# Kernel tuning notes

Hardware: AMD Instinct MI355X
Metric: run time of the kernel (lower is better)

The kernel has to match this reference:

```python
import jax, jax.numpy as jnp
import numpy as np
from jax import lax


def setup_inputs() -> dict:
    key = jax.random.key(0)
    k1, k2 = jax.random.split(key)
    x = jax.random.normal(k1, (16, 224, 224, 256), dtype=jnp.float32)
    # Conv2D(1, 7): kernel HWIO [7,7,2,1], glorot-ish scale
    conv_w = jax.random.normal(k2, (7, 7, 2, 1), dtype=jnp.float32) * 0.1
    conv_b = jnp.zeros((1,), dtype=jnp.float32)
    return {"x": x, "conv_w": conv_w, "conv_b": conv_b}


def reference(x, conv_w, conv_b):
    # channel-wise stats: [B,H,W,1] each
    max_pool = jnp.max(x, axis=-1, keepdims=True)
    avg_pool = jnp.mean(x, axis=-1, keepdims=True)
    concat = jnp.concatenate([max_pool, avg_pool], axis=-1)  # [B,H,W,2]
    attn = lax.conv_general_dilated(
        concat, conv_w,
        window_strides=(1, 1), padding='SAME',
        dimension_numbers=('NHWC', 'HWIO', 'NHWC'))
    attn = jax.nn.sigmoid(attn + conv_b)  # [B,H,W,1]
    return x * attn
```

## Files before the change

kernel.cpp:

```cpp
#include <hip/hip_runtime.h>
#include <math.h>

#define B_ 16
#define H_ 224
#define W_ 224
#define C_ 256
#define NPIX (B_*H_*W_)
#define NROW (B_*H_)

typedef float f32x4 __attribute__((ext_vector_type(4)));

__global__ __launch_bounds__(256) void pool_kernel(const float* __restrict__ x,
                                                   float2* __restrict__ pooled) {
    const int t    = threadIdx.x;
    const int wave = t >> 6;
    const int lane = t & 63;
    const int grp  = lane >> 4;
    const int sub  = lane & 15;
    const int pid  = (blockIdx.x * 4 + wave) * 4 + grp;
    const f32x4* px = (const f32x4*)(x + (size_t)pid * C_);
    float m = -INFINITY, s = 0.0f;
    #pragma unroll
    for (int j = 0; j < 4; ++j) {
        f32x4 v = __builtin_nontemporal_load(&px[j * 16 + sub]);
        m = fmaxf(m, fmaxf(fmaxf(v.x, v.y), fmaxf(v.z, v.w)));
        s += (v.x + v.y) + (v.z + v.w);
    }
    #pragma unroll
    for (int off = 1; off < 16; off <<= 1) {
        m = fmaxf(m, __shfl_xor(m, off));
        s += __shfl_xor(s, off);
    }
    if (sub == 0) pooled[pid] = make_float2(m, s * (1.0f / 256.0f));
}

__global__ __launch_bounds__(256) void attn_row_kernel(const float* __restrict__ x,
                                                       const float2* __restrict__ pooled,
                                                       const float* __restrict__ cw,
                                                       const float* __restrict__ cb,
                                                       float* __restrict__ out) {
    __shared__ float2 spool[7][232];
    __shared__ float2 sw2[49];
    __shared__ float  sbias;
    __shared__ float  sattn[224];

    const int t   = threadIdx.x;
    const int bid = blockIdx.x;
    const int row = (bid & 7) * (NROW / 8) + (bid >> 3);
    const int b   = row / H_;
    const int h   = row % H_;

    if (t < 98)  ((float*)sw2)[t] = cw[t];
    if (t == 98) sbias = cb[0];

    const float2* prow = pooled + (size_t)b * (H_ * W_);
    for (int idx = t; idx < 7 * 230; idx += 256) {
        const int r  = idx / 230;
        const int ci = idx % 230;
        const int hh = h - 3 + r;
        const int c  = ci - 3;
        float2 v = make_float2(0.0f, 0.0f);
        if (hh >= 0 && hh < H_ && c >= 0 && c < W_) v = prow[hh * W_ + c];
        spool[r][ci] = v;
    }
    __syncthreads();

    if (t < W_) {
        float acc = 0.0f;
        #pragma unroll
        for (int kh = 0; kh < 7; ++kh) {
            #pragma unroll
            for (int kw = 0; kw < 7; ++kw) {
                const float2 pv = spool[kh][t + kw];
                const float2 wv = sw2[kh * 7 + kw];
                acc = fmaf(pv.x, wv.x, fmaf(pv.y, wv.y, acc));
            }
        }
        sattn[t] = 1.0f / (1.0f + expf(-(acc + sbias)));
    }
    __syncthreads();

    const f32x4* xx = (const f32x4*)(x   + (size_t)row * W_ * C_);
    f32x4*       oo = (f32x4*)      (out + (size_t)row * W_ * C_);
    #pragma unroll 4
    for (int i = 0; i < 56; ++i) {
        const int idx = i * 256 + t;
        const float a = sattn[idx >> 6];
        f32x4 v = __builtin_nontemporal_load(&xx[idx]);
        v.x *= a; v.y *= a; v.z *= a; v.w *= a;
        __builtin_nontemporal_store(v, &oo[idx]);
    }
}

extern "C" void kernel_launch(void* const* d_in, const int* in_sizes, int n_in,
                              void* d_out, int out_size, void* d_ws, size_t ws_size,
                              hipStream_t stream) {
    const float* x  = (const float*)d_in[0];
    const float* cw = (const float*)d_in[1];
    const float* cb = (const float*)d_in[2];
    float* out      = (float*)d_out;
    float2* pooled  = (float2*)d_ws;

    pool_kernel<<<NPIX / 16, 256, 0, stream>>>(x, pooled);
    attn_row_kernel<<<NROW, 256, 0, stream>>>(x, pooled, cw, cb, out);
}
```

Baseline: 435.8 us.

## Software-pipeline pooling and multiply per image to keep x resident in cache

Replaces the two full-tensor passes with 17 launches of one combined kernel. Each launch pools image d while applying attention to image d-1, so x for the previous image (about 51 MB) can still be in the large last-level cache when it is read a second time. Loads switch from nontemporal to normal so the data is kept in cache. The cost is 17 launches with their boundaries and tail effects, plus a per-launch split of blocks between the two roles.

```diff
diff --git a/kernel.cpp b/kernel.cpp
--- a/kernel.cpp
+++ b/kernel.cpp
@@ -5,90 +5,99 @@
 #define H_ 224
 #define W_ 224
 #define C_ 256
-#define NPIX (B_*H_*W_)
-#define NROW (B_*H_)
+#define IMGPIX (H_*W_)
+#define MULB 448
+#define POOLB 1568
+#define GRID (MULB + POOLB)
 
 typedef float f32x4 __attribute__((ext_vector_type(4)));
 
-__global__ __launch_bounds__(256) void pool_kernel(const float* __restrict__ x,
-                                                   float2* __restrict__ pooled) {
-    const int t    = threadIdx.x;
-    const int wave = t >> 6;
-    const int lane = t & 63;
-    const int grp  = lane >> 4;
-    const int sub  = lane & 15;
-    const int pid  = (blockIdx.x * 4 + wave) * 4 + grp;
-    const f32x4* px = (const f32x4*)(x + (size_t)pid * C_);
-    float m = -INFINITY, s = 0.0f;
-    #pragma unroll
-    for (int j = 0; j < 4; ++j) {
-        f32x4 v = __builtin_nontemporal_load(&px[j * 16 + sub]);
-        m = fmaxf(m, fmaxf(fmaxf(v.x, v.y), fmaxf(v.z, v.w)));
-        s += (v.x + v.y) + (v.z + v.w);
-    }
-    #pragma unroll
-    for (int off = 1; off < 16; off <<= 1) {
-        m = fmaxf(m, __shfl_xor(m, off));
-        s += __shfl_xor(s, off);
-    }
-    if (sub == 0) pooled[pid] = make_float2(m, s * (1.0f / 256.0f));
-}
-
-__global__ __launch_bounds__(256) void attn_row_kernel(const float* __restrict__ x,
-                                                       const float2* __restrict__ pooled,
-                                                       const float* __restrict__ cw,
-                                                       const float* __restrict__ cb,
-                                                       float* __restrict__ out) {
-    __shared__ float2 spool[7][232];
-    __shared__ float2 sw2[49];
-    __shared__ float  sbias;
-    __shared__ float  sattn[224];
-
+__global__ __launch_bounds__(256) void step_kernel(const float* __restrict__ x,
+                                                   const float* __restrict__ cw,
+                                                   const float* __restrict__ cb,
+                                                   float* __restrict__ out,
+                                                   float2* __restrict__ pooled,
+                                                   int mb, int pb) {
     const int t   = threadIdx.x;
     const int bid = blockIdx.x;
-    const int row = (bid & 7) * (NROW / 8) + (bid >> 3);
-    const int b   = row / H_;
-    const int h   = row % H_;
 
-    if (t < 98)  ((float*)sw2)[t] = cw[t];
-    if (t == 98) sbias = cb[0];
+    if (bid < MULB) {
+        if (mb < 0) return;
+        __shared__ float2 spool[7][118];
+        __shared__ float2 sw2[49];
+        __shared__ float  sbias;
+        __shared__ float  sattn[112];
 
-    const float2* prow = pooled + (size_t)b * (H_ * W_);
-    for (int idx = t; idx < 7 * 230; idx += 256) {
-        const int r  = idx / 230;
-        const int ci = idx % 230;
-        const int hh = h - 3 + r;
-        const int c  = ci - 3;
-        float2 v = make_float2(0.0f, 0.0f);
-        if (hh >= 0 && hh < H_ && c >= 0 && c < W_) v = prow[hh * W_ + c];
-        spool[r][ci] = v;
-    }
-    __syncthreads();
+        const int row  = bid >> 1;
+        const int col0 = (bid & 1) * 112;
 
-    if (t < W_) {
-        float acc = 0.0f;
+        if (t < 98)  ((float*)sw2)[t] = cw[t];
+        if (t == 98) sbias = cb[0];
+
+        const float2* pbase = pooled + (size_t)mb * IMGPIX;
+        for (int idx = t; idx < 7 * 118; idx += 256) {
+            const int r  = idx / 118;
+            const int ci = idx % 118;
+            const int hh = row - 3 + r;
+            const int c  = col0 - 3 + ci;
+            float2 v = make_float2(0.0f, 0.0f);
+            if (hh >= 0 && hh < H_ && c >= 0 && c < W_) v = pbase[hh * W_ + c];
+            spool[r][ci] = v;
+        }
+        __syncthreads();
+
+        if (t < 112) {
+            float acc = 0.0f;
+            #pragma unroll
+            for (int kh = 0; kh < 7; ++kh) {
+                #pragma unroll
+                for (int kw = 0; kw < 7; ++kw) {
+                    const float2 pv = spool[kh][t + kw];
+                    const float2 wv = sw2[kh * 7 + kw];
+                    acc = fmaf(pv.x, wv.x, fmaf(pv.y, wv.y, acc));
+                }
+            }
+            sattn[t] = 1.0f / (1.0f + expf(-(acc + sbias)));
+        }
+        __syncthreads();
+
+        const size_t pix0 = (size_t)mb * IMGPIX + (size_t)row * W_ + col0;
+        const f32x4* xx = (const f32x4*)x   + pix0 * 64;
+        f32x4*       oo = (f32x4*)out + pix0 * 64;
+        #pragma unroll 4
+        for (int i = 0; i < 28; ++i) {
+            const int idx = i * 256 + t;
+            const float a = sattn[idx >> 6];
+            f32x4 v = xx[idx];
+            v.x *= a; v.y *= a; v.z *= a; v.w *= a;
+            __builtin_nontemporal_store(v, &oo[idx]);
+        }
+    } else {
+        if (pb < 0) return;
+        const int pp  = bid - MULB;
+        const int px0 = pp * 32;
+        const int g   = t >> 4;
+        const int sub = t & 15;
+        const float*  xb  = x + (size_t)pb * IMGPIX * C_;
+        float2*       pot = pooled + (size_t)pb * IMGPIX;
         #pragma unroll
-        for (int kh = 0; kh < 7; ++kh) {
+        for (int pi = 0; pi < 2; ++pi) {
+            const int px = px0 + pi * 16 + g;
+            const f32x4* p4 = (const f32x4*)(xb + (size_t)px * C_);
+            float m = -INFINITY, s = 0.0f;
             #pragma unroll
-            for (int kw = 0; kw < 7; ++kw) {
-                const float2 pv = spool[kh][t + kw];
-                const float2 wv = sw2[kh * 7 + kw];
-                acc = fmaf(pv.x, wv.x, fmaf(pv.y, wv.y, acc));
+            for (int j = 0; j < 4; ++j) {
+                f32x4 v = p4[j * 16 + sub];
+                m = fmaxf(m, fmaxf(fmaxf(v.x, v.y), fmaxf(v.z, v.w)));
+                s += (v.x + v.y) + (v.z + v.w);
             }
+            #pragma unroll
+            for (int off = 1; off < 16; off <<= 1) {
+                m = fmaxf(m, __shfl_xor(m, off));
+                s += __shfl_xor(s, off);
+            }
+            if (sub == 0) pot[px] = make_float2(m, s * (1.0f / 256.0f));
         }
-        sattn[t] = 1.0f / (1.0f + expf(-(acc + sbias)));
-    }
-    __syncthreads();
-
-    const f32x4* xx = (const f32x4*)(x   + (size_t)row * W_ * C_);
-    f32x4*       oo = (f32x4*)      (out + (size_t)row * W_ * C_);
-    #pragma unroll 4
-    for (int i = 0; i < 56; ++i) {
-        const int idx = i * 256 + t;
-        const float a = sattn[idx >> 6];
-        f32x4 v = __builtin_nontemporal_load(&xx[idx]);
-        v.x *= a; v.y *= a; v.z *= a; v.w *= a;
-        __builtin_nontemporal_store(v, &oo[idx]);
     }
 }
 
@@ -101,6 +110,9 @@
     float* out      = (float*)d_out;
     float2* pooled  = (float2*)d_ws;
 
-    pool_kernel<<<NPIX / 16, 256, 0, stream>>>(x, pooled);
-    attn_row_kernel<<<NROW, 256, 0, stream>>>(x, pooled, cw, cb, out);
+    for (int d = 0; d <= B_; ++d) {
+        const int mb = d - 1;
+        const int pb = (d < B_) ? d : -1;
+        step_kernel<<<GRID, 256, 0, stream>>>(x, cw, cb, out, pooled, mb, pb);
+    }
 }
```

Result: faster. 415.8 us (-4.6%).
